# Kernel tuning notes

Hardware: AMD Instinct MI355X
Metric: run time of the kernel (lower is better)

Reference implementation:

```python
import jax, jax.numpy as jnp
import numpy as np

N = 20000
DEG = 16
E = N * DEG
IN_DIM = 512
OUT_DIM = 512
H = 4
D = OUT_DIM // H            # head_dim = 128
POS_DIM = 3
M_ROPE = D // (POS_DIM * 2) # 21
D_ROPE = POS_DIM * 2 * M_ROPE  # 126 (2 trailing dims unrotated)
ROPE_BASE = 10000.0

INV_FREQ = jnp.exp(-jnp.arange(M_ROPE, dtype=jnp.float32) * (np.log(ROPE_BASE) / M_ROPE))


def _rope(t, pos):
    # t: (N, D, H), pos: (N, POS_DIM)
    n = t.shape[0]
    angles = pos[:, :, None] * INV_FREQ[None, None, :]        # (N, POS_DIM, M)
    cos = jnp.cos(angles)[..., None]                           # (N, POS_DIM, M, 1)
    sin = jnp.sin(angles)[..., None]
    part = t[:, :D_ROPE, :].reshape(n, POS_DIM, M_ROPE, 2, H)
    even, odd = part[..., 0, :], part[..., 1, :]
    rot_even = even * cos - odd * sin
    rot_odd = even * sin + odd * cos
    rot = jnp.stack((rot_even, rot_odd), axis=3).reshape(n, D_ROPE, H)
    return jnp.concatenate([rot, t[:, D_ROPE:, :]], axis=1)


def setup_inputs() -> dict:
    key = jax.random.key(0)
    ks = jax.random.split(key, 12)
    x = jax.random.normal(ks[0], (N, IN_DIM), jnp.float32)
    pos = jax.random.uniform(ks[1], (N, POS_DIM), jnp.float32) * 100.0
    rows = jnp.repeat(jnp.arange(N, dtype=jnp.int32), DEG)  # sorted, every node has DEG out-edges
    cols = jax.random.randint(ks[2], (E,), 0, N, dtype=jnp.int32)
    s = 1.0 / np.sqrt(IN_DIM)
    Wq = jax.random.normal(ks[3], (OUT_DIM, IN_DIM), jnp.float32) * s
    Wk = jax.random.normal(ks[4], (OUT_DIM, IN_DIM), jnp.float32) * s
    Wv = jax.random.normal(ks[5], (OUT_DIM, IN_DIM), jnp.float32) * s
    Wo = jax.random.normal(ks[6], (OUT_DIM, OUT_DIM), jnp.float32) * s
    bq = jax.random.normal(ks[7], (OUT_DIM,), jnp.float32) * 0.01
    bk = jax.random.normal(ks[8], (OUT_DIM,), jnp.float32) * 0.01
    bv = jax.random.normal(ks[9], (OUT_DIM,), jnp.float32) * 0.01
    bo = jax.random.normal(ks[10], (OUT_DIM,), jnp.float32) * 0.01
    return {"x": x, "pos": pos, "rows": rows, "cols": cols,
            "Wq": Wq, "bq": bq, "Wk": Wk, "bk": bk, "Wv": Wv, "bv": bv, "Wo": Wo, "bo": bo}


def reference(x, pos, rows, cols, Wq, bq, Wk, bk, Wv, bv, Wo, bo):
    n = x.shape[0]
    q = (x @ Wq.T + bq).reshape(n, D, H)
    k = (x @ Wk.T + bk).reshape(n, D, H)
    v = (x @ Wv.T + bv).reshape(n, D, H)
    # scaling by sqrt(k.size(1)) == sqrt(head_dim)
    q = q / jnp.sqrt(jnp.asarray(D, q.dtype))
    q = _rope(q, pos)
    k = _rope(k, pos)
    # per-edge scores: s[e,h] = sum_d q[rows[e],d,h] * k[cols[e],d,h]
    scores = jnp.einsum('edh,edh->eh', q[rows], k[cols])  # (E, H)
    # row-wise sparse softmax per head
    row_max = jax.ops.segment_max(scores, rows, num_segments=n, indices_are_sorted=True)
    p = jnp.exp(scores - row_max[rows])
    denom = jax.ops.segment_sum(p, rows, num_segments=n, indices_are_sorted=True)
    attn = p / denom[rows]                                 # (E, H)
    # bspmm: y[i,d,h] = sum_{e: rows[e]=i} attn[e,h] * v[cols[e],d,h]
    y = jax.ops.segment_sum(attn[:, None, :] * v[cols], rows, num_segments=n, indices_are_sorted=True)
    out = y.reshape(n, OUT_DIM) @ Wo.T + bo
    return out
```

## Files before the change

kernel.cpp:

```cpp
#include <hip/hip_runtime.h>
#include <hip/hip_bf16.h>

#define NN 20000
#define DEG 16
#define KD 512
#define OD 512
#define NH 4
#define DH 128
#define DROPE 126

#define BM 128
#define BN 128
#define BK 64

typedef unsigned short u16;
typedef unsigned int u32;
typedef __attribute__((ext_vector_type(8))) short short8;
typedef __attribute__((ext_vector_type(4))) float f32x4;

__device__ __forceinline__ float b2f(u16 u){ return __uint_as_float((u32)u << 16); }
__device__ __forceinline__ u16 f2b(float f){
  u32 x = __float_as_uint(f);
  return (u16)((x + 0x7fffu + ((x >> 16) & 1u)) >> 16);
}
__device__ __forceinline__ void up8(uint4 u, float* f){
  f[0]=__uint_as_float(u.x<<16); f[1]=__uint_as_float(u.x&0xffff0000u);
  f[2]=__uint_as_float(u.y<<16); f[3]=__uint_as_float(u.y&0xffff0000u);
  f[4]=__uint_as_float(u.z<<16); f[5]=__uint_as_float(u.z&0xffff0000u);
  f[6]=__uint_as_float(u.w<<16); f[7]=__uint_as_float(u.w&0xffff0000u);
}
__device__ __forceinline__ uint4 cvt8(const float* s){
  uint4 a = *(const uint4*)s;
  uint4 b = *(const uint4*)(s + 4);
  uint4 o;
  o.x = (u32)f2b(__uint_as_float(a.x)) | ((u32)f2b(__uint_as_float(a.y)) << 16);
  o.y = (u32)f2b(__uint_as_float(a.z)) | ((u32)f2b(__uint_as_float(a.w)) << 16);
  o.z = (u32)f2b(__uint_as_float(b.x)) | ((u32)f2b(__uint_as_float(b.y)) << 16);
  o.w = (u32)f2b(__uint_as_float(b.z)) | ((u32)f2b(__uint_as_float(b.w)) << 16);
  return o;
}

__device__ __forceinline__ void load_lds16(const u16* g, u16* l) {
  __builtin_amdgcn_global_load_lds(
      (const __attribute__((address_space(1))) void*)g,
      (__attribute__((address_space(3))) void*)l, 16, 0, 0);
}

struct ConvJob {
  const float* x;  u16* xb;
  const float* w[4]; u16* wb[4];
  const float* b[4]; u16* bb[4];
};
__global__ __launch_bounds__(256) void conv_all(ConvJob j) {
  const int b = blockIdx.x;
  if (b < 5000) {
    const int i8 = (b * 256 + threadIdx.x) * 8;
    *(uint4*)(j.xb + i8) = cvt8(j.x + i8);
  } else if (b < 5512) {
    const int t = b - 5000;
    const int wsel = t >> 7;
    const int i8 = ((t & 127) * 256 + threadIdx.x) * 8;
    if (wsel < 3) {
      *(uint4*)(j.wb[wsel] + i8) = cvt8(j.w[wsel] + i8);
    } else {
      const int o = i8 >> 9, cp = i8 & 511;
      const int h = cp >> 7, d0 = cp & 127;
      const float* src = j.w[3] + (size_t)o * 512 + h;
      float tmp[8];
      #pragma unroll
      for (int t2 = 0; t2 < 8; t2++) tmp[t2] = src[(size_t)(d0 + t2) * 4];
      uint4 ov;
      ov.x = (u32)f2b(tmp[0]) | ((u32)f2b(tmp[1]) << 16);
      ov.y = (u32)f2b(tmp[2]) | ((u32)f2b(tmp[3]) << 16);
      ov.z = (u32)f2b(tmp[4]) | ((u32)f2b(tmp[5]) << 16);
      ov.w = (u32)f2b(tmp[6]) | ((u32)f2b(tmp[7]) << 16);
      *(uint4*)(j.wb[3] + i8) = ov;
    }
  } else {
    const int vsel = threadIdx.x >> 6;
    const int i8 = (threadIdx.x & 63) * 8;
    *(uint4*)(j.bb[vsel] + i8) = cvt8(j.b[vsel] + i8);
  }
}

__global__ __launch_bounds__(256, 2) void gemm_k(
    const u16* __restrict__ A,
    const u16* __restrict__ W0, const u16* __restrict__ B0,
    const u16* __restrict__ W1, const u16* __restrict__ B1,
    const u16* __restrict__ W2, const u16* __restrict__ B2,
    const float* __restrict__ pos,
    u16* __restrict__ o0, u16* __restrict__ o1, void* __restrict__ o2,
    int M, int only2, int f32out)
{
  __shared__ __align__(16) char smem[65536];
  __shared__ float posS[BM*3];
  __shared__ float freqS[21];

  const int b = blockIdx.x;
  const int xcd = b & 7, rem = b >> 3;
  int rowT, colT, w;
  if (only2) {
    rowT = (rem >> 2)*8 + xcd; colT = rem & 3; w = 2;
  } else {
    rowT = (rem / 12)*8 + xcd; const int sub = rem % 12; colT = sub & 3; w = sub >> 2;
  }
  if (rowT*BM >= M) return;

  const int tid = threadIdx.x;
  const int wave = tid >> 6, lane = tid & 63;
  const int wr = wave >> 1, wc = wave & 1;
  const int lm = lane & 15, lq = lane >> 4;
  const u16* W  = (w == 0) ? W0 : ((w == 1) ? W1 : W2);
  const u16* Bi = (w == 0) ? B0 : ((w == 1) ? B1 : B2);
  const int emode = only2 ? 3 : w;
  u16* outQKV = (w == 0) ? o0 : ((w == 1) ? o1 : (u16*)o2);

  f32x4 acc[4][4];
  #pragma unroll
  for (int i = 0; i < 4; i++)
    #pragma unroll
    for (int jj = 0; jj < 4; jj++)
      acc[i][jj] = (f32x4){0.f, 0.f, 0.f, 0.f};

  if (emode < 2) {
    if (tid < BM) {
      int gr = rowT*BM + tid; if (gr >= M) gr = M - 1;
      posS[tid*3+0] = pos[gr*3+0];
      posS[tid*3+1] = pos[gr*3+1];
      posS[tid*3+2] = pos[gr*3+2];
    }
    if (tid >= BM && tid < BM + 21)
      freqS[tid - BM] = __expf(-(float)(tid - BM) * 0.43858763676077064f);
  }
  __builtin_amdgcn_sched_barrier(0);
  asm volatile("s_waitcnt vmcnt(0)" ::: "memory");

  auto stage = [&](int bufi, int kt) {
    u16* Asb = (u16*)(smem + bufi*32768);
    u16* Bsb = Asb + BM*BK;
    #pragma unroll
    for (int it = 0; it < 4; it++) {
      const int chunk = it*256 + wave*64 + lane;
      const int row = chunk >> 3, gseg = (chunk & 7) ^ (row & 7);
      int gr = rowT*BM + row; if (gr >= M) gr = M - 1;
      load_lds16(A + (size_t)gr*KD + kt + gseg*8,
                 Asb + (size_t)(it*256 + wave*64)*8);
    }
    #pragma unroll
    for (int it = 0; it < 4; it++) {
      const int chunk = it*256 + wave*64 + lane;
      const int row = chunk >> 3, gseg = (chunk & 7) ^ (row & 7);
      load_lds16(W + (size_t)(colT*BN + row)*KD + kt + gseg*8,
                 Bsb + (size_t)(it*256 + wave*64)*8);
    }
  };

  stage(0, 0);

  for (int t = 0; t < 8; t++) {
    const int cur = t & 1;
    if (t < 7) stage(cur ^ 1, (t + 1) * BK);
    __builtin_amdgcn_sched_barrier(0);
    if (t < 7) asm volatile("s_waitcnt vmcnt(8)" ::: "memory");
    else       asm volatile("s_waitcnt vmcnt(0)" ::: "memory");
    __builtin_amdgcn_s_barrier();
    __builtin_amdgcn_sched_barrier(0);

    const u16* Asb = (const u16*)(smem + cur*32768);
    const u16* Bsb = Asb + BM*BK;
    #pragma unroll
    for (int kk = 0; kk < BK; kk += 32) {
      const int ks = kk >> 3;
      short8 af[4], bfr[4];
      #pragma unroll
      for (int i = 0; i < 4; i++) {
        const int ra = wr*64 + i*16 + lm;
        af[i] = *(const short8*)(Asb + (size_t)(ra*8 + ((ks + lq) ^ (ra & 7)))*8);
      }
      #pragma unroll
      for (int i = 0; i < 4; i++) {
        const int rb = wc*64 + i*16 + lm;
        bfr[i] = *(const short8*)(Bsb + (size_t)(rb*8 + ((ks + lq) ^ (rb & 7)))*8);
      }
      #pragma unroll
      for (int mi = 0; mi < 4; mi++)
        #pragma unroll
        for (int ni = 0; ni < 4; ni++)
          acc[mi][ni] = __builtin_amdgcn_mfma_f32_16x16x32_bf16(af[mi], bfr[ni], acc[mi][ni], 0, 0, 0);
    }
    __builtin_amdgcn_sched_barrier(0);
    __builtin_amdgcn_s_barrier();
  }

  float bvv[4];
  #pragma unroll
  for (int ni = 0; ni < 4; ni++)
    bvv[ni] = b2f(Bi[colT*BN + wc*64 + ni*16 + lm]);

  u16* Cs = (u16*)smem;

  if (emode == 3) {
    #pragma unroll
    for (int mi = 0; mi < 4; mi++)
      #pragma unroll
      for (int ni = 0; ni < 4; ni++) {
        const int Cg = colT*BN + wc*64 + ni*16 + lm;
        #pragma unroll
        for (int r = 0; r < 4; r++) {
          const int grow = rowT*BM + wr*64 + mi*16 + lq*4 + r;
          if (grow < M) ((float*)o2)[(size_t)grow*OD + Cg] = acc[mi][ni][r] + bvv[ni];
        }
      }
    return;
  }

  #pragma unroll
  for (int mi = 0; mi < 4; mi++) {
    #pragma unroll
    for (int ni = 0; ni < 4; ni++) {
      const int cloc = wc*64 + ni*16 + lm;
      const int h = cloc & 3, dloc = cloc >> 2;
      const int d = colT*32 + dloc;
      #pragma unroll
      for (int r = 0; r < 4; r++) {
        const int rloc = wr*64 + mi*16 + lq*4 + r;
        float v = acc[mi][ni][r] + bvv[ni];
        if (emode == 0) v *= 0.08838834764831845f;
        float vr = v;
        if (emode < 2) {
          const float partner = __shfl_xor(v, 4);
          if (d < DROPE) {
            const int pp = d / 42, rem2 = d - pp*42, m = rem2 >> 1, par = rem2 & 1;
            const float ang = posS[rloc*3 + pp] * freqS[m];
            float sn, cs; __sincosf(ang, &sn, &cs);
            vr = par ? (v*cs + partner*sn) : (v*cs - partner*sn);
          }
        }
        Cs[rloc*144 + h*36 + dloc] = f2b(vr);
      }
    }
  }
  __syncthreads();
  #pragma unroll
  for (int pass = 0; pass < 8; pass++) {
    const int c2 = pass*256 + tid;
    const int dd8 = c2 & 3, h = (c2 >> 2) & 3, rloc = c2 >> 4;
    const int grow = rowT*BM + rloc;
    if (grow < M) {
      uint2 a = *(const uint2*)(Cs + rloc*144 + h*36 + dd8*8);
      uint2 b2 = *(const uint2*)(Cs + rloc*144 + h*36 + dd8*8 + 4);
      *(uint4*)(outQKV + ((size_t)grow*NH + h)*DH + colT*32 + dd8*8)
          = make_uint4(a.x, a.y, b2.x, b2.y);
    }
  }
}

__global__ __launch_bounds__(256, 3) void edge_attn(
    const int* __restrict__ cols, const u16* __restrict__ qf,
    const u16* __restrict__ kf, const u16* __restrict__ vf,
    u16* __restrict__ y)
{
  const int b = blockIdx.x;
  const int xcd = b & 7;
  const int head = xcd >> 1;
  const int nbase = (b >> 3) * 32 + (xcd & 1) * 16;
  const int wave = threadIdx.x >> 6, lane = threadIdx.x & 63;
  const int g = lane >> 4, l16 = lane & 15;
  const int n = nbase + wave*4 + g;

  const int col = cols[n*DEG + l16];
  const uint4 qv = *(const uint4*)(qf + ((size_t)n*NH + head)*DH + l16*8);

  uint4 kreg[16];
  #pragma unroll
  for (int jj = 0; jj < 16; jj++) {
    const int cj = __shfl(col, g*16 + jj);
    kreg[jj] = *(const uint4*)(kf + ((size_t)cj*NH + head)*DH + l16*8);
  }
  float qa[8]; up8(qv, qa);

  float s = 0.f;
  #pragma unroll
  for (int jj = 0; jj < 16; jj++) {
    float ka[8]; up8(kreg[jj], ka);
    float pr = qa[0]*ka[0] + qa[1]*ka[1] + qa[2]*ka[2] + qa[3]*ka[3]
             + qa[4]*ka[4] + qa[5]*ka[5] + qa[6]*ka[6] + qa[7]*ka[7];
    pr += __shfl_xor(pr, 1);
    pr += __shfl_xor(pr, 2);
    pr += __shfl_xor(pr, 4);
    pr += __shfl_xor(pr, 8);
    s = (l16 == jj) ? pr : s;
  }

  float mx = s;
  #pragma unroll
  for (int msk = 1; msk < 16; msk <<= 1) mx = fmaxf(mx, __shfl_xor(mx, msk));
  float p = expf(s - mx);
  float dn = p;
  #pragma unroll
  for (int msk = 1; msk < 16; msk <<= 1) dn += __shfl_xor(dn, msk);
  const float attn = p / dn;

  uint4 vreg[16];
  #pragma unroll
  for (int jj = 0; jj < 16; jj++) {
    const int cj = __shfl(col, g*16 + jj);
    vreg[jj] = *(const uint4*)(vf + ((size_t)cj*NH + head)*DH + l16*8);
  }
  float ya[8];
  #pragma unroll
  for (int t = 0; t < 8; t++) ya[t] = 0.f;
  #pragma unroll
  for (int jj = 0; jj < 16; jj++) {
    const float a = __shfl(attn, g*16 + jj);
    float va[8]; up8(vreg[jj], va);
    #pragma unroll
    for (int t = 0; t < 8; t++) ya[t] += a*va[t];
  }
  u32 pk[4];
  #pragma unroll
  for (int t = 0; t < 4; t++)
    pk[t] = (u32)f2b(ya[2*t]) | ((u32)f2b(ya[2*t+1]) << 16);
  *(uint4*)(y + ((size_t)n*NH + head)*DH + l16*8) = make_uint4(pk[0], pk[1], pk[2], pk[3]);
}

extern "C" void kernel_launch(void* const* d_in, const int* in_sizes, int n_in,
                              void* d_out, int out_size, void* d_ws, size_t ws_size,
                              hipStream_t stream) {
  (void)in_sizes; (void)n_in; (void)out_size; (void)ws_size;
  const float* x   = (const float*)d_in[0];
  const float* pos = (const float*)d_in[1];
  const int* cols = (const int*)d_in[3];
  const float* Wq = (const float*)d_in[4];
  const float* bq = (const float*)d_in[5];
  const float* Wk = (const float*)d_in[6];
  const float* bk = (const float*)d_in[7];
  const float* Wv = (const float*)d_in[8];
  const float* bv = (const float*)d_in[9];
  const float* Wo = (const float*)d_in[10];
  const float* bo = (const float*)d_in[11];

  char* ws = (char*)d_ws;
  size_t off = 0;
  auto carve = [&](size_t bytes) { char* p = ws + off; off += (bytes + 15) & ~(size_t)15; return p; };
  u16* xb   = (u16*)carve((size_t)NN*KD*2);
  u16* Wqb  = (u16*)carve((size_t)OD*KD*2);
  u16* Wkb  = (u16*)carve((size_t)OD*KD*2);
  u16* Wvb  = (u16*)carve((size_t)OD*KD*2);
  u16* Wob  = (u16*)carve((size_t)OD*OD*2);
  u16* bqb  = (u16*)carve((size_t)OD*2);
  u16* bkb  = (u16*)carve((size_t)OD*2);
  u16* bvb  = (u16*)carve((size_t)OD*2);
  u16* bob  = (u16*)carve((size_t)OD*2);
  u16* qf   = (u16*)carve((size_t)NN*OD*2);
  u16* kf   = (u16*)carve((size_t)NN*OD*2);
  u16* vf   = (u16*)carve((size_t)NN*OD*2);
  u16* y    = (u16*)carve((size_t)NN*OD*2);

  ConvJob cj;
  cj.x = x; cj.xb = xb;
  cj.w[0]=Wq; cj.w[1]=Wk; cj.w[2]=Wv; cj.w[3]=Wo;
  cj.wb[0]=Wqb; cj.wb[1]=Wkb; cj.wb[2]=Wvb; cj.wb[3]=Wob;
  cj.b[0]=bq; cj.b[1]=bk; cj.b[2]=bv; cj.b[3]=bo;
  cj.bb[0]=bqb; cj.bb[1]=bkb; cj.bb[2]=bvb; cj.bb[3]=bob;
  conv_all<<<dim3(5513), 256, 0, stream>>>(cj);

  gemm_k<<<dim3(1920), 256, 0, stream>>>(xb, Wqb, bqb, Wkb, bkb, Wvb, bvb, pos,
                                         qf, kf, (void*)vf, NN, 0, 0);
  edge_attn<<<dim3(5000), 256, 0, stream>>>(cols, qf, kf, vf, y);
  gemm_k<<<dim3(640), 256, 0, stream>>>(y, Wqb, bqb, Wkb, bkb, Wob, bob, pos,
                                        qf, kf, d_out, NN, 1, 1);
}
```

Baseline: 258.3 us.

## Split edge attention into score and gather kernels, add dedicated output GEMM

```diff
diff --git a/kernel.cpp b/kernel.cpp
--- a/kernel.cpp
+++ b/kernel.cpp
@@ -89,8 +89,8 @@
     const u16* __restrict__ W1, const u16* __restrict__ B1,
     const u16* __restrict__ W2, const u16* __restrict__ B2,
     const float* __restrict__ pos,
-    u16* __restrict__ o0, u16* __restrict__ o1, void* __restrict__ o2,
-    int M, int only2, int f32out)
+    u16* __restrict__ o0, u16* __restrict__ o1, u16* __restrict__ o2,
+    int M)
 {
   __shared__ __align__(16) char smem[65536];
   __shared__ float posS[BM*3];
@@ -98,12 +98,9 @@
 
   const int b = blockIdx.x;
   const int xcd = b & 7, rem = b >> 3;
-  int rowT, colT, w;
-  if (only2) {
-    rowT = (rem >> 2)*8 + xcd; colT = rem & 3; w = 2;
-  } else {
-    rowT = (rem / 12)*8 + xcd; const int sub = rem % 12; colT = sub & 3; w = sub >> 2;
-  }
+  const int rowT = (rem / 12)*8 + xcd;
+  const int sub = rem % 12;
+  const int colT = sub & 3, w = sub >> 2;
   if (rowT*BM >= M) return;
 
   const int tid = threadIdx.x;
@@ -112,8 +109,8 @@
   const int lm = lane & 15, lq = lane >> 4;
   const u16* W  = (w == 0) ? W0 : ((w == 1) ? W1 : W2);
   const u16* Bi = (w == 0) ? B0 : ((w == 1) ? B1 : B2);
-  const int emode = only2 ? 3 : w;
-  u16* outQKV = (w == 0) ? o0 : ((w == 1) ? o1 : (u16*)o2);
+  const int emode = w;
+  u16* outQKV = (w == 0) ? o0 : ((w == 1) ? o1 : o2);
 
   f32x4 acc[4][4];
   #pragma unroll
@@ -198,21 +195,6 @@
     bvv[ni] = b2f(Bi[colT*BN + wc*64 + ni*16 + lm]);
 
   u16* Cs = (u16*)smem;
-
-  if (emode == 3) {
-    #pragma unroll
-    for (int mi = 0; mi < 4; mi++)
-      #pragma unroll
-      for (int ni = 0; ni < 4; ni++) {
-        const int Cg = colT*BN + wc*64 + ni*16 + lm;
-        #pragma unroll
-        for (int r = 0; r < 4; r++) {
-          const int grow = rowT*BM + wr*64 + mi*16 + lq*4 + r;
-          if (grow < M) ((float*)o2)[(size_t)grow*OD + Cg] = acc[mi][ni][r] + bvv[ni];
-        }
-      }
-    return;
-  }
 
   #pragma unroll
   for (int mi = 0; mi < 4; mi++) {
@@ -255,10 +237,92 @@
   }
 }
 
-__global__ __launch_bounds__(256, 3) void edge_attn(
+__global__ __launch_bounds__(256, 4) void gemm_o(
+    const u16* __restrict__ A, const u16* __restrict__ W,
+    const u16* __restrict__ Bi, float* __restrict__ out, int M)
+{
+  __shared__ __align__(16) u16 As[BM*BK];
+  __shared__ __align__(16) u16 Bs[BN*BK];
+
+  const int b = blockIdx.x;
+  const int xcd = b & 7, rem = b >> 3;
+  const int rowT = (rem >> 2)*8 + xcd, colT = rem & 3;
+  if (rowT*BM >= M) return;
+
+  const int tid = threadIdx.x;
+  const int wave = tid >> 6, lane = tid & 63;
+  const int wr = wave >> 1, wc = wave & 1;
+  const int lm = lane & 15, lq = lane >> 4;
+
+  f32x4 acc[4][4];
+  #pragma unroll
+  for (int i = 0; i < 4; i++)
+    #pragma unroll
+    for (int jj = 0; jj < 4; jj++)
+      acc[i][jj] = (f32x4){0.f, 0.f, 0.f, 0.f};
+
+  for (int kt = 0; kt < KD; kt += BK) {
+    #pragma unroll
+    for (int it = 0; it < 4; it++) {
+      const int chunk = it*256 + wave*64 + lane;
+      const int row = chunk >> 3, gseg = (chunk & 7) ^ (row & 7);
+      int gr = rowT*BM + row; if (gr >= M) gr = M - 1;
+      load_lds16(A + (size_t)gr*KD + kt + gseg*8,
+                 As + (size_t)(it*256 + wave*64)*8);
+    }
+    #pragma unroll
+    for (int it = 0; it < 4; it++) {
+      const int chunk = it*256 + wave*64 + lane;
+      const int row = chunk >> 3, gseg = (chunk & 7) ^ (row & 7);
+      load_lds16(W + (size_t)(colT*BN + row)*KD + kt + gseg*8,
+                 Bs + (size_t)(it*256 + wave*64)*8);
+    }
+    __syncthreads();
+    #pragma unroll
+    for (int kk = 0; kk < BK; kk += 32) {
+      const int ks = kk >> 3;
+      short8 af[4], bfr[4];
+      #pragma unroll
+      for (int i = 0; i < 4; i++) {
+        const int ra = wr*64 + i*16 + lm;
+        af[i] = *(const short8*)(As + (size_t)(ra*8 + ((ks + lq) ^ (ra & 7)))*8);
+      }
+      #pragma unroll
+      for (int i = 0; i < 4; i++) {
+        const int rb = wc*64 + i*16 + lm;
+        bfr[i] = *(const short8*)(Bs + (size_t)(rb*8 + ((ks + lq) ^ (rb & 7)))*8);
+      }
+      #pragma unroll
+      for (int mi = 0; mi < 4; mi++)
+        #pragma unroll
+        for (int ni = 0; ni < 4; ni++)
+          acc[mi][ni] = __builtin_amdgcn_mfma_f32_16x16x32_bf16(af[mi], bfr[ni], acc[mi][ni], 0, 0, 0);
+    }
+    __syncthreads();
+  }
+
+  float bvv[4];
+  #pragma unroll
+  for (int ni = 0; ni < 4; ni++)
+    bvv[ni] = b2f(Bi[colT*BN + wc*64 + ni*16 + lm]);
+
+  #pragma unroll
+  for (int mi = 0; mi < 4; mi++)
+    #pragma unroll
+    for (int ni = 0; ni < 4; ni++) {
+      const int Cg = colT*BN + wc*64 + ni*16 + lm;
+      #pragma unroll
+      for (int r = 0; r < 4; r++) {
+        const int grow = rowT*BM + wr*64 + mi*16 + lq*4 + r;
+        if (grow < M) out[(size_t)grow*OD + Cg] = acc[mi][ni][r] + bvv[ni];
+      }
+    }
+}
+
+
+__global__ __launch_bounds__(256, 3) void edge_score(
     const int* __restrict__ cols, const u16* __restrict__ qf,
-    const u16* __restrict__ kf, const u16* __restrict__ vf,
-    u16* __restrict__ y)
+    const u16* __restrict__ kf, float* __restrict__ aw)
 {
   const int b = blockIdx.x;
   const int xcd = b & 7;
@@ -299,7 +363,23 @@
   float dn = p;
   #pragma unroll
   for (int msk = 1; msk < 16; msk <<= 1) dn += __shfl_xor(dn, msk);
-  const float attn = p / dn;
+  aw[(size_t)(n*NH + head)*DEG + l16] = p / dn;
+}
+
+__global__ __launch_bounds__(256, 3) void edge_gather(
+    const int* __restrict__ cols, const u16* __restrict__ vf,
+    const float* __restrict__ aw, u16* __restrict__ y)
+{
+  const int b = blockIdx.x;
+  const int xcd = b & 7;
+  const int head = xcd >> 1;
+  const int nbase = (b >> 3) * 32 + (xcd & 1) * 16;
+  const int wave = threadIdx.x >> 6, lane = threadIdx.x & 63;
+  const int g = lane >> 4, l16 = lane & 15;
+  const int n = nbase + wave*4 + g;
+
+  const int col = cols[n*DEG + l16];
+  const float a_l = aw[(size_t)(n*NH + head)*DEG + l16];
 
   uint4 vreg[16];
   #pragma unroll
@@ -307,12 +387,13 @@
     const int cj = __shfl(col, g*16 + jj);
     vreg[jj] = *(const uint4*)(vf + ((size_t)cj*NH + head)*DH + l16*8);
   }
+
   float ya[8];
   #pragma unroll
   for (int t = 0; t < 8; t++) ya[t] = 0.f;
   #pragma unroll
   for (int jj = 0; jj < 16; jj++) {
-    const float a = __shfl(attn, g*16 + jj);
+    const float a = __shfl(a_l, g*16 + jj);
     float va[8]; up8(vreg[jj], va);
     #pragma unroll
     for (int t = 0; t < 8; t++) ya[t] += a*va[t];
@@ -356,6 +437,7 @@
   u16* kf   = (u16*)carve((size_t)NN*OD*2);
   u16* vf   = (u16*)carve((size_t)NN*OD*2);
   u16* y    = (u16*)carve((size_t)NN*OD*2);
+  float* aw = (float*)carve((size_t)NN*NH*DEG*4);
 
   ConvJob cj;
   cj.x = x; cj.xb = xb;
@@ -366,8 +448,8 @@
   conv_all<<<dim3(5513), 256, 0, stream>>>(cj);
 
   gemm_k<<<dim3(1920), 256, 0, stream>>>(xb, Wqb, bqb, Wkb, bkb, Wvb, bvb, pos,
-                                         qf, kf, (void*)vf, NN, 0, 0);
-  edge_attn<<<dim3(5000), 256, 0, stream>>>(cols, qf, kf, vf, y);
-  gemm_k<<<dim3(640), 256, 0, stream>>>(y, Wqb, bqb, Wkb, bkb, Wob, bob, pos,
-                                        qf, kf, d_out, NN, 1, 1);
-}
+                                         qf, kf, vf, NN);
+  edge_score<<<dim3(5000), 256, 0, stream>>>(cols, qf, kf, aw);
+  edge_gather<<<dim3(5000), 256, 0, stream>>>(cols, vf, aw, y);
+  gemm_o<<<dim3(640), 256, 0, stream>>>(y, Wob, bob, (float*)d_out, NN);
+}
```

After: 237.5 us. 1.09x faster.
